# Performance work log

Hardware: AMD Instinct MI355X
Metric: run time of the kernel (lower is better)

## Reference

```python
import jax, jax.numpy as jnp
import numpy as np
from jax import lax

MAX_DECAY = 0.99
EPS = 1e-05
TOPK = 4


def ema_mask_group(moving_avg, new, mask, decay0, cluster_update_num):
    """Faithful port of ema_tensor_mask_group_inplace, including the quirk that
    the Python-level `decay` variable is carried (and possibly shrunk) across
    cluster iterations. Implemented as a lax.scan over clusters carrying decay.
    moving_avg/new: [C] or [C, D]; mask, cluster_update_num: [C].
    """
    def step(decay, xs):
        ma, nw, m, c = xs
        d = jnp.where((m != 0) & (c <= 10.0), decay * c / 10.0, decay)
        out = jnp.where(m != 0, ma * d + nw * (1.0 - d), ma)
        return d, out
    _, out = lax.scan(step, jnp.asarray(decay0, moving_avg.dtype),
                      (moving_avg, new, mask, cluster_update_num))
    return out


def laplace_smoothing(x, n_categories, eps=EPS):
    return (x + eps) / (x.sum() + n_categories * eps)


def setup_inputs() -> dict:
    key = jax.random.key(0)
    k1, k2 = jax.random.split(key)
    N, C, D = 65536, 512, 256
    return {
        "inputs_flatten": jax.random.normal(k1, (N, D), dtype=jnp.float32),
        "dictionary": jax.random.normal(k2, (C, D), dtype=jnp.float32),
        "cluster_size_sum": jnp.zeros((C,), dtype=jnp.float32),
        "cluster_value": jnp.zeros((C, D), dtype=jnp.float32),
        "cluster_update_num": jnp.ones((C,), dtype=jnp.float32),
    }


def reference(inputs_flatten, dictionary, cluster_size_sum, cluster_value,
              cluster_update_num):
    N, D = inputs_flatten.shape
    C = dictionary.shape[0]
    dic = lax.stop_gradient(dictionary)  # dictionary used via .detach()/.data

    # squared euclidean distances [N, C]
    distances = (jnp.sum(inputs_flatten ** 2, axis=1, keepdims=True)
                 + jnp.sum(dic ** 2, axis=1)
                 - 2.0 * jnp.matmul(inputs_flatten, dic.T))

    # ascending sort -> take topK smallest distances
    _, topk_idx = lax.top_k(-distances, TOPK)          # [N, K]
    topk_emb = dic[topk_idx]                            # [N, K, D]
    group_emb = jnp.sum(topk_emb, axis=1) / TOPK        # [N, D]

    # multi-hot encodings via scatter
    rows = jnp.arange(N)[:, None]
    encodings = jnp.zeros((N, C), dtype=jnp.float32).at[rows, topk_idx].set(1.0)

    # ---- training-mode EMA codebook update (single device: all_gather = identity) ----
    x_sg = lax.stop_gradient(inputs_flatten)
    cluster_size = jnp.sum(encodings, axis=0)           # [C]
    cluster_mask = (cluster_size != 0).astype(jnp.float32)
    cluster_update_num_new = cluster_update_num + cluster_mask

    cluster_size_sum_new = ema_mask_group(cluster_size_sum, cluster_size,
                                          cluster_mask, MAX_DECAY,
                                          cluster_update_num_new)
    input_sum = jnp.matmul(encodings.T, x_sg)           # [C, D]
    cluster_value_new = ema_mask_group(cluster_value, input_sum, cluster_mask,
                                       MAX_DECAY, cluster_update_num_new)

    cs = laplace_smoothing(cluster_size_sum_new, C, EPS) * cluster_size_sum_new.sum()
    embed_normalized = jnp.where(cluster_mask[:, None] == 1.0,
                                 cluster_value_new / cs[:, None],
                                 cluster_value_new)
    dictionary_new = embed_normalized                   # world_size == 1

    # straight-through estimator
    group_emb = lax.stop_gradient(group_emb - inputs_flatten) + inputs_flatten
    return (group_emb, topk_idx, dictionary_new, cluster_size_sum_new,
            cluster_value_new, cluster_update_num_new)
```

## Files before the change

kernel.cpp:

```cpp
#include <hip/hip_runtime.h>

#define N_ROWS 65536
#define C_CLUST 512
#define D_DIM 256

#define WS_DICTT   0
#define WS_DSQ     131072
#define WS_CS      197120
#define WS_DCY     197632
#define WS_ISUM    198144
#define WS_COUNTS  329216
#define WS_OFFSETS 329728
#define WS_FILL    330752
#define WS_ROWLIST 331264

#define OUT_GEMB 0
#define OUT_TOPK 16777216
#define OUT_DICT 17039360
#define OUT_CSS  17170432
#define OUT_CV   17170944
#define OUT_CNUM 17302016

#define RPB 128

typedef __attribute__((ext_vector_type(8))) short short8;
typedef __attribute__((ext_vector_type(16))) float f32x16;

__device__ __forceinline__ unsigned short f2bf(float v) {
    union { float f; unsigned u; } c; c.f = v;
    unsigned r = c.u + 0x7FFFu + ((c.u >> 16) & 1u);
    return (unsigned short)(r >> 16);
}
__device__ __forceinline__ float bf2f(unsigned short h) {
    union { float f; unsigned u; } c; c.u = ((unsigned)h) << 16;
    return c.f;
}

__global__ void zero_k(unsigned* counts, unsigned* fill, float* isum) {
    int t = blockIdx.x * blockDim.x + threadIdx.x;
    if (t < 512) { counts[t] = 0u; fill[t] = 0u; }
    if (t < C_CLUST * D_DIM) isum[t] = 0.f;
}

__global__ void prep_dict(const float* __restrict__ dic, float* __restrict__ ws) {
    int c = blockIdx.x, k = threadIdx.x;
    float v = dic[c * D_DIM + k];
    unsigned short* dhi = (unsigned short*)(ws + WS_DICTT);
    unsigned short* dlo = dhi + 131072;
    unsigned short hb = f2bf(v);
    dhi[c * D_DIM + k] = hb;
    dlo[c * D_DIM + k] = f2bf(__fsub_rn(v, bf2f(hb)));
    __shared__ float red[256];
    red[k] = v * v;
    __syncthreads();
    for (int s = 128; s > 0; s >>= 1) {
        if (k < s) red[k] += red[k + s];
        __syncthreads();
    }
    if (k == 0) ws[WS_DSQ + c] = red[0];
}

__global__ __launch_bounds__(256, 2) void stage1_cand(
    const float* __restrict__ x, const float* __restrict__ ws,
    float* __restrict__ cand_out)
{
    __shared__ unsigned short hlds[32 * 264];
    __shared__ unsigned short llds[32 * 264];
    __shared__ float dsq_s[512];

    const int tid = threadIdx.x;
    const int lane = tid & 63;
    const int w = tid >> 6;
    const int kg = lane >> 5;
    const int cl_lane = lane & 31;
    const int row = blockIdx.x * 128 + w * 32 + cl_lane;

    const unsigned short* dhi = (const unsigned short*)(ws + WS_DICTT);
    const unsigned short* dlo = dhi + 131072;

    for (int i = tid; i < 512; i += 256) dsq_s[i] = ws[WS_DSQ + i];

    short8 bhi[16], blo[16];
    #pragma unroll
    for (int s = 0; s < 16; ++s) {
        const float* px = &x[(size_t)row * D_DIM + s * 16 + kg * 8];
        float4 u0 = *reinterpret_cast<const float4*>(px);
        float4 u1 = *reinterpret_cast<const float4*>(px + 4);
        float vv[8] = {u0.x, u0.y, u0.z, u0.w, u1.x, u1.y, u1.z, u1.w};
        short8 h, l;
        #pragma unroll
        for (int e = 0; e < 8; ++e) {
            unsigned short hb = f2bf(vv[e]);
            unsigned short lb = f2bf(__fsub_rn(vv[e], bf2f(hb)));
            h[e] = (short)hb; l[e] = (short)lb;
        }
        bhi[s] = h; blo[s] = l;
    }

    unsigned long long kk[8];
    #pragma unroll
    for (int q = 0; q < 8; ++q) kk[q] = 0xFFFFFFFFFFFFFFFFULL;

    for (int ct = 0; ct < 16; ++ct) {
        __syncthreads();
        for (int q = tid; q < 1024; q += 256) {
            int c = q >> 5, k8 = (q & 31) * 8;
            *reinterpret_cast<uint4*>(&hlds[c * 264 + k8]) =
                *reinterpret_cast<const uint4*>(&dhi[(ct * 32 + c) * D_DIM + k8]);
            *reinterpret_cast<uint4*>(&llds[c * 264 + k8]) =
                *reinterpret_cast<const uint4*>(&dlo[(ct * 32 + c) * D_DIM + k8]);
        }
        __syncthreads();

        f32x16 ahh, ahl, alh;
        #pragma unroll
        for (int r = 0; r < 16; ++r) { ahh[r] = 0.f; ahl[r] = 0.f; alh[r] = 0.f; }

        #pragma unroll
        for (int s = 0; s < 16; ++s) {
            short8 Ah = *reinterpret_cast<const short8*>(
                &hlds[cl_lane * 264 + s * 16 + kg * 8]);
            short8 Al = *reinterpret_cast<const short8*>(
                &llds[cl_lane * 264 + s * 16 + kg * 8]);
            ahh = __builtin_amdgcn_mfma_f32_32x32x16_bf16(Ah, bhi[s], ahh, 0, 0, 0);
            ahl = __builtin_amdgcn_mfma_f32_32x32x16_bf16(Ah, blo[s], ahl, 0, 0, 0);
            alh = __builtin_amdgcn_mfma_f32_32x32x16_bf16(Al, bhi[s], alh, 0, 0, 0);
        }

        #pragma unroll
        for (int r = 0; r < 16; ++r) {
            int cl = ct * 32 + (r & 3) + 8 * (r >> 2) + 4 * kg;
            float dot = ahh[r] + ahl[r] + alh[r];
            float key = (dsq_s[cl] + 1024.0f) - 2.0f * dot;
            unsigned long long v =
                ((unsigned long long)__float_as_uint(key) << 32) | (unsigned)cl;
            #pragma unroll
            for (int q = 0; q < 8; ++q) {
                bool lt = v < kk[q];
                unsigned long long mn = lt ? v : kk[q];
                unsigned long long mx = lt ? kk[q] : v;
                kk[q] = mn; v = mx;
            }
        }
    }

    uint4 wv;
    wv.x = (unsigned)(kk[0] & 0xFFFF) | ((unsigned)(kk[1] & 0xFFFF) << 16);
    wv.y = (unsigned)(kk[2] & 0xFFFF) | ((unsigned)(kk[3] & 0xFFFF) << 16);
    wv.z = (unsigned)(kk[4] & 0xFFFF) | ((unsigned)(kk[5] & 0xFFFF) << 16);
    wv.w = (unsigned)(kk[6] & 0xFFFF) | ((unsigned)(kk[7] & 0xFFFF) << 16);
    *reinterpret_cast<uint4*>(&cand_out[(size_t)row * 256 + kg * 4]) = wv;
}

__global__ __launch_bounds__(256, 2) void refine_k(
    const float* __restrict__ x, const float* __restrict__ dic,
    const float* __restrict__ ws, float* __restrict__ out,
    unsigned* __restrict__ counts)
{
    extern __shared__ float smem[];
    float* xl  = smem;
    float* dl  = smem + 4 * 260;
    float* sqb = smem + 4 * 260 + 64 * 260;
    __shared__ float distb[64];
    __shared__ float xss[4];
    __shared__ int cidx[64];
    __shared__ int selp[16];

    const int t = threadIdx.x;
    const int rowBase = blockIdx.x * 4;
    const unsigned short* candp = (const unsigned short*)(out + OUT_GEMB);

    if (t < 64) cidx[t] = (int)candp[(size_t)(rowBase + (t >> 4)) * 512 + (t & 15)];

    {
        int r = t >> 6, seg = t & 63;
        const float* px = &x[(size_t)(rowBase + r) * D_DIM + seg * 4];
        float4 a = *reinterpret_cast<const float4*>(px);
        *reinterpret_cast<float4*>(&xl[r * 260 + seg * 4]) = a;
        sqb[r * 256 + seg * 4 + 0] = a.x * a.x;
        sqb[r * 256 + seg * 4 + 1] = a.y * a.y;
        sqb[r * 256 + seg * 4 + 2] = a.z * a.z;
        sqb[r * 256 + seg * 4 + 3] = a.w * a.w;
    }
    __syncthreads();

    {
        int r = t >> 6, g = t & 63;
        for (int st = 128; st > 0; st >>= 1) {
            for (int k = g; k < st; k += 64)
                sqb[r * 256 + k] += sqb[r * 256 + k + st];
            __syncthreads();
        }
        if (t < 4) xss[t] = sqb[t * 256];
    }
    __syncthreads();

    {
        int p = t >> 2, q = t & 3;
        const float* src = &dic[(size_t)cidx[p] * D_DIM + q * 64];
        #pragma unroll
        for (int i = 0; i < 16; ++i)
            *reinterpret_cast<float4*>(&dl[p * 260 + q * 64 + i * 4]) =
                *reinterpret_cast<const float4*>(src + i * 4);
    }
    __syncthreads();

    if (t < 64) {
        int r = t >> 4;
        float acc = 0.f;
        const float* dp = &dl[t * 260];
        const float* xp = &xl[r * 260];
        #pragma unroll 4
        for (int k4 = 0; k4 < 64; ++k4) {
            float4 dv = *reinterpret_cast<const float4*>(dp + k4 * 4);
            float4 xv = *reinterpret_cast<const float4*>(xp + k4 * 4);
            acc = fmaf(xv.x, dv.x, acc);
            acc = fmaf(xv.y, dv.y, acc);
            acc = fmaf(xv.z, dv.z, acc);
            acc = fmaf(xv.w, dv.w, acc);
        }
        float ds = ws[WS_DSQ + cidx[t]];
        distb[t] = __fsub_rn(__fadd_rn(xss[r], ds), __fmul_rn(2.0f, acc));
    }
    __syncthreads();

    if (t < 4) {
        float bv0 = 3.4e38f, bv1 = 3.4e38f, bv2 = 3.4e38f, bv3 = 3.4e38f;
        int bi0 = 0x7FFFFFFF, bi1 = 0x7FFFFFFF, bi2 = 0x7FFFFFFF, bi3 = 0x7FFFFFFF;
        int bp0 = 0, bp1 = 0, bp2 = 0, bp3 = 0;
        for (int s = 0; s < 16; ++s) {
            int p = t * 16 + s;
            float v = distb[p];
            int ci = cidx[p];
            if (v < bv3 || (v == bv3 && ci < bi3)) {
                if (v < bv2 || (v == bv2 && ci < bi2)) {
                    bv3 = bv2; bi3 = bi2; bp3 = bp2;
                    if (v < bv1 || (v == bv1 && ci < bi1)) {
                        bv2 = bv1; bi2 = bi1; bp2 = bp1;
                        if (v < bv0 || (v == bv0 && ci < bi0)) {
                            bv1 = bv0; bi1 = bi0; bp1 = bp0;
                            bv0 = v; bi0 = ci; bp0 = p;
                        } else { bv1 = v; bi1 = ci; bp1 = p; }
                    } else { bv2 = v; bi2 = ci; bp2 = p; }
                } else { bv3 = v; bi3 = ci; bp3 = p; }
            }
        }
        int row = rowBase + t;
        out[OUT_TOPK + (size_t)row * 4 + 0] = (float)bi0;
        out[OUT_TOPK + (size_t)row * 4 + 1] = (float)bi1;
        out[OUT_TOPK + (size_t)row * 4 + 2] = (float)bi2;
        out[OUT_TOPK + (size_t)row * 4 + 3] = (float)bi3;
        atomicAdd(&counts[bi0], 1u);
        atomicAdd(&counts[bi1], 1u);
        atomicAdd(&counts[bi2], 1u);
        atomicAdd(&counts[bi3], 1u);
        selp[t * 4 + 0] = bp0 & 63;
        selp[t * 4 + 1] = bp1 & 63;
        selp[t * 4 + 2] = bp2 & 63;
        selp[t * 4 + 3] = bp3 & 63;
    }
    __syncthreads();

    {
        int r = t >> 6, u = t & 63;
        int p0 = selp[r * 4 + 0], p1 = selp[r * 4 + 1];
        int p2 = selp[r * 4 + 2], p3 = selp[r * 4 + 3];
        int k4 = u * 4;
        float4 a = *reinterpret_cast<const float4*>(&dl[p0 * 260 + k4]);
        float4 b = *reinterpret_cast<const float4*>(&dl[p1 * 260 + k4]);
        float4 c = *reinterpret_cast<const float4*>(&dl[p2 * 260 + k4]);
        float4 e = *reinterpret_cast<const float4*>(&dl[p3 * 260 + k4]);
        float4 xv = *reinterpret_cast<const float4*>(&xl[r * 260 + k4]);
        float4 o;
        float g;
        g = __fmul_rn(__fadd_rn(__fadd_rn(__fadd_rn(a.x, b.x), c.x), e.x), 0.25f);
        o.x = __fadd_rn(__fsub_rn(g, xv.x), xv.x);
        g = __fmul_rn(__fadd_rn(__fadd_rn(__fadd_rn(a.y, b.y), c.y), e.y), 0.25f);
        o.y = __fadd_rn(__fsub_rn(g, xv.y), xv.y);
        g = __fmul_rn(__fadd_rn(__fadd_rn(__fadd_rn(a.z, b.z), c.z), e.z), 0.25f);
        o.z = __fadd_rn(__fsub_rn(g, xv.z), xv.z);
        g = __fmul_rn(__fadd_rn(__fadd_rn(__fadd_rn(a.w, b.w), c.w), e.w), 0.25f);
        o.w = __fadd_rn(__fsub_rn(g, xv.w), xv.w);
        *reinterpret_cast<float4*>(
            &out[OUT_GEMB + (size_t)(rowBase + r) * D_DIM + k4]) = o;
    }
}

__global__ void prefix_k(const unsigned* __restrict__ counts, unsigned* __restrict__ offsets) {
    __shared__ unsigned s[512];
    int t = threadIdx.x;
    unsigned my = counts[t];
    s[t] = my;
    __syncthreads();
    for (int off = 1; off < 512; off <<= 1) {
        unsigned v = (t >= off) ? s[t - off] : 0u;
        __syncthreads();
        s[t] += v;
        __syncthreads();
    }
    offsets[t] = s[t] - my;
    if (t == 511) offsets[512] = s[511];
}

__global__ void scatter_k(const float* __restrict__ topk, const unsigned* __restrict__ offsets,
                          unsigned* __restrict__ fill, unsigned* __restrict__ rowlist) {
    int row = blockIdx.x * 256 + threadIdx.x;
    #pragma unroll
    for (int k = 0; k < 4; ++k) {
        int c = (int)topk[row * 4 + k];
        unsigned p = atomicAdd(&fill[c], 1u);
        rowlist[offsets[c] + p] = ((unsigned)c << 16) | (unsigned)row;
    }
}

__global__ __launch_bounds__(256, 8) void cluster_sum2_k(
    const float* __restrict__ x, const unsigned* __restrict__ rowlist,
    float* __restrict__ isum)
{
    const int d = threadIdx.x;
    const int base = blockIdx.x * RPB;
    unsigned e0 = rowlist[base];
    int ccur = (int)(e0 >> 16);
    float acc = 0.f;
    #pragma unroll 4
    for (int j = 0; j < RPB; ++j) {
        unsigned e = rowlist[base + j];
        int c = (int)(e >> 16);
        float v = x[(e & 0xFFFFu) * D_DIM + d];
        if (c != ccur) {
            atomicAdd(&isum[ccur * D_DIM + d], acc);
            acc = 0.f;
            ccur = c;
        }
        acc += v;
    }
    atomicAdd(&isum[ccur * D_DIM + d], acc);
}

__global__ void ema_scalar_k(const float* __restrict__ css_in, const float* __restrict__ cnum_in,
                             const unsigned* __restrict__ counts,
                             float* __restrict__ ws, float* __restrict__ out) {
    __shared__ float sdecay[512];
    __shared__ float sred[512];
    __shared__ float scn[512];
    __shared__ unsigned smask[512];
    int t = threadIdx.x;
    unsigned cnt = counts[t];
    float size = (float)cnt;
    float mask = (cnt != 0u) ? 1.f : 0.f;
    float cnum_new = __fadd_rn(cnum_in[t], mask);
    scn[t] = cnum_new;
    smask[t] = cnt;
    __syncthreads();
    if (t == 0) {
        float d = 0.99f;
        for (int c = 0; c < 512; ++c) {
            if (smask[c] != 0u && scn[c] <= 10.0f)
                d = __fmul_rn(d, scn[c]) / 10.0f;
            sdecay[c] = d;
        }
    }
    __syncthreads();
    float d = sdecay[t];
    float css = css_in[t];
    float css_new = (cnt != 0u)
        ? __fadd_rn(__fmul_rn(css, d), __fmul_rn(size, __fsub_rn(1.f, d)))
        : css;
    out[OUT_CSS + t] = css_new;
    out[OUT_CNUM + t] = cnum_new;
    sred[t] = css_new;
    __syncthreads();
    for (int s = 256; s > 0; s >>= 1) {
        if (t < s) sred[t] += sred[t + s];
        __syncthreads();
    }
    float S = sred[0];
    float cs = __fmul_rn(__fdiv_rn(__fadd_rn(css_new, 1e-5f),
                                   __fadd_rn(S, 0.00512f)), S);
    ws[WS_CS + t] = cs;
    ws[WS_DCY + t] = d;
}

__global__ void final_k(const float* __restrict__ cv_in, const float* __restrict__ ws,
                        const unsigned* __restrict__ counts, float* __restrict__ out) {
    int c = blockIdx.x, d = threadIdx.x;
    float isum = ws[WS_ISUM + c * D_DIM + d];
    float dc = ws[WS_DCY + c];
    float cs = ws[WS_CS + c];
    unsigned cnt = counts[c];
    float cv = cv_in[c * D_DIM + d];
    float cvn = (cnt != 0u)
        ? __fadd_rn(__fmul_rn(cv, dc), __fmul_rn(isum, __fsub_rn(1.f, dc)))
        : cv;
    out[OUT_CV + c * D_DIM + d] = cvn;
    out[OUT_DICT + c * D_DIM + d] = (cnt != 0u) ? __fdiv_rn(cvn, cs) : cvn;
}

extern "C" void kernel_launch(void* const* d_in, const int* in_sizes, int n_in,
                              void* d_out, int out_size, void* d_ws, size_t ws_size,
                              hipStream_t stream) {
    const float* x       = (const float*)d_in[0];
    const float* dic     = (const float*)d_in[1];
    const float* css_in  = (const float*)d_in[2];
    const float* cv_in   = (const float*)d_in[3];
    const float* cnum_in = (const float*)d_in[4];
    float* out = (float*)d_out;
    float* ws  = (float*)d_ws;
    unsigned* counts  = (unsigned*)(ws + WS_COUNTS);
    unsigned* offsets = (unsigned*)(ws + WS_OFFSETS);
    unsigned* fill    = (unsigned*)(ws + WS_FILL);
    unsigned* rowlist = (unsigned*)(ws + WS_ROWLIST);

    zero_k<<<C_CLUST * D_DIM / 256, 256, 0, stream>>>(counts, fill, ws + WS_ISUM);
    prep_dict<<<C_CLUST, 256, 0, stream>>>(dic, ws);

    stage1_cand<<<N_ROWS / 128, 256, 0, stream>>>(x, ws, out + OUT_GEMB);

    size_t smem2 = (4 * 260 + 64 * 260 + 4 * 256) * sizeof(float);
    refine_k<<<N_ROWS / 4, 256, smem2, stream>>>(x, dic, ws, out, counts);

    prefix_k<<<1, 512, 0, stream>>>(counts, offsets);
    scatter_k<<<N_ROWS / 256, 256, 0, stream>>>(out + OUT_TOPK, offsets, fill, rowlist);
    cluster_sum2_k<<<N_ROWS * 4 / RPB, 256, 0, stream>>>(x, rowlist, ws + WS_ISUM);
    ema_scalar_k<<<1, 512, 0, stream>>>(css_in, cnum_in, counts, ws, out);
    final_k<<<C_CLUST, 256, 0, stream>>>(cv_in, ws, counts, out);
}
```

Measured before the change: 673.2 us.

## Restructure refine kernel to 16 rows per block with precomputed row norms

```diff
diff --git a/kernel.cpp b/kernel.cpp
--- a/kernel.cpp
+++ b/kernel.cpp
@@ -6,6 +6,7 @@
 
 #define WS_DICTT   0
 #define WS_DSQ     131072
+#define WS_XSQ     131584
 #define WS_CS      197120
 #define WS_DCY     197632
 #define WS_ISUM    198144
@@ -58,6 +59,19 @@
         __syncthreads();
     }
     if (k == 0) ws[WS_DSQ + c] = red[0];
+}
+
+__global__ void row_sq(const float* __restrict__ x, float* __restrict__ ws) {
+    int row = blockIdx.x, k = threadIdx.x;
+    float v = x[row * D_DIM + k];
+    __shared__ float red[256];
+    red[k] = v * v;
+    __syncthreads();
+    for (int s = 128; s > 0; s >>= 1) {
+        if (k < s) red[k] += red[k + s];
+        __syncthreads();
+    }
+    if (k == 0) ws[WS_XSQ + row] = red[0];
 }
 
 __global__ __launch_bounds__(256, 2) void stage1_cand(
@@ -152,65 +166,39 @@
     *reinterpret_cast<uint4*>(&cand_out[(size_t)row * 256 + kg * 4]) = wv;
 }
 
-__global__ __launch_bounds__(256, 2) void refine_k(
+__global__ __launch_bounds__(256, 4) void refine_k(
     const float* __restrict__ x, const float* __restrict__ dic,
     const float* __restrict__ ws, float* __restrict__ out,
     unsigned* __restrict__ counts)
 {
-    extern __shared__ float smem[];
-    float* xl  = smem;
-    float* dl  = smem + 4 * 260;
-    float* sqb = smem + 4 * 260 + 64 * 260;
-    __shared__ float distb[64];
-    __shared__ float xss[4];
-    __shared__ int cidx[64];
-    __shared__ int selp[16];
+    __shared__ float xl[16 * 260];
+    __shared__ float distb[256];
+    __shared__ int cidx[256];
+    __shared__ int seli[16 * 4];
 
     const int t = threadIdx.x;
-    const int rowBase = blockIdx.x * 4;
+    const int rowBase = blockIdx.x * 16;
     const unsigned short* candp = (const unsigned short*)(out + OUT_GEMB);
 
-    if (t < 64) cidx[t] = (int)candp[(size_t)(rowBase + (t >> 4)) * 512 + (t & 15)];
+    cidx[t] = (int)candp[(size_t)(rowBase + (t >> 4)) * 512 + (t & 15)];
+
+    #pragma unroll
+    for (int i = 0; i < 4; ++i) {
+        int q = t + i * 256;
+        int r = q >> 6, seg = q & 63;
+        *reinterpret_cast<float4*>(&xl[r * 260 + seg * 4]) =
+            *reinterpret_cast<const float4*>(
+                &x[(size_t)(rowBase + r) * D_DIM + seg * 4]);
+    }
+    __syncthreads();
 
     {
-        int r = t >> 6, seg = t & 63;
-        const float* px = &x[(size_t)(rowBase + r) * D_DIM + seg * 4];
-        float4 a = *reinterpret_cast<const float4*>(px);
-        *reinterpret_cast<float4*>(&xl[r * 260 + seg * 4]) = a;
-        sqb[r * 256 + seg * 4 + 0] = a.x * a.x;
-        sqb[r * 256 + seg * 4 + 1] = a.y * a.y;
-        sqb[r * 256 + seg * 4 + 2] = a.z * a.z;
-        sqb[r * 256 + seg * 4 + 3] = a.w * a.w;
-    }
-    __syncthreads();
-
-    {
-        int r = t >> 6, g = t & 63;
-        for (int st = 128; st > 0; st >>= 1) {
-            for (int k = g; k < st; k += 64)
-                sqb[r * 256 + k] += sqb[r * 256 + k + st];
-            __syncthreads();
-        }
-        if (t < 4) xss[t] = sqb[t * 256];
-    }
-    __syncthreads();
-
-    {
-        int p = t >> 2, q = t & 3;
-        const float* src = &dic[(size_t)cidx[p] * D_DIM + q * 64];
-        #pragma unroll
-        for (int i = 0; i < 16; ++i)
-            *reinterpret_cast<float4*>(&dl[p * 260 + q * 64 + i * 4]) =
-                *reinterpret_cast<const float4*>(src + i * 4);
-    }
-    __syncthreads();
-
-    if (t < 64) {
         int r = t >> 4;
+        int ci = cidx[t];
+        const float* dp = &dic[(size_t)ci * D_DIM];
+        const float* xp = &xl[r * 260];
         float acc = 0.f;
-        const float* dp = &dl[t * 260];
-        const float* xp = &xl[r * 260];
-        #pragma unroll 4
+        #pragma unroll 8
         for (int k4 = 0; k4 < 64; ++k4) {
             float4 dv = *reinterpret_cast<const float4*>(dp + k4 * 4);
             float4 xv = *reinterpret_cast<const float4*>(xp + k4 * 4);
@@ -219,30 +207,30 @@
             acc = fmaf(xv.z, dv.z, acc);
             acc = fmaf(xv.w, dv.w, acc);
         }
-        float ds = ws[WS_DSQ + cidx[t]];
-        distb[t] = __fsub_rn(__fadd_rn(xss[r], ds), __fmul_rn(2.0f, acc));
-    }
-    __syncthreads();
-
-    if (t < 4) {
+        float ds = ws[WS_DSQ + ci];
+        float xs = ws[WS_XSQ + rowBase + r];
+        distb[t] = __fsub_rn(__fadd_rn(xs, ds), __fmul_rn(2.0f, acc));
+    }
+    __syncthreads();
+
+    if (t < 16) {
         float bv0 = 3.4e38f, bv1 = 3.4e38f, bv2 = 3.4e38f, bv3 = 3.4e38f;
         int bi0 = 0x7FFFFFFF, bi1 = 0x7FFFFFFF, bi2 = 0x7FFFFFFF, bi3 = 0x7FFFFFFF;
-        int bp0 = 0, bp1 = 0, bp2 = 0, bp3 = 0;
         for (int s = 0; s < 16; ++s) {
             int p = t * 16 + s;
             float v = distb[p];
             int ci = cidx[p];
             if (v < bv3 || (v == bv3 && ci < bi3)) {
                 if (v < bv2 || (v == bv2 && ci < bi2)) {
-                    bv3 = bv2; bi3 = bi2; bp3 = bp2;
+                    bv3 = bv2; bi3 = bi2;
                     if (v < bv1 || (v == bv1 && ci < bi1)) {
-                        bv2 = bv1; bi2 = bi1; bp2 = bp1;
+                        bv2 = bv1; bi2 = bi1;
                         if (v < bv0 || (v == bv0 && ci < bi0)) {
-                            bv1 = bv0; bi1 = bi0; bp1 = bp0;
-                            bv0 = v; bi0 = ci; bp0 = p;
-                        } else { bv1 = v; bi1 = ci; bp1 = p; }
-                    } else { bv2 = v; bi2 = ci; bp2 = p; }
-                } else { bv3 = v; bi3 = ci; bp3 = p; }
+                            bv1 = bv0; bi1 = bi0;
+                            bv0 = v; bi0 = ci;
+                        } else { bv1 = v; bi1 = ci; }
+                    } else { bv2 = v; bi2 = ci; }
+                } else { bv3 = v; bi3 = ci; }
             }
         }
         int row = rowBase + t;
@@ -254,35 +242,38 @@
         atomicAdd(&counts[bi1], 1u);
         atomicAdd(&counts[bi2], 1u);
         atomicAdd(&counts[bi3], 1u);
-        selp[t * 4 + 0] = bp0 & 63;
-        selp[t * 4 + 1] = bp1 & 63;
-        selp[t * 4 + 2] = bp2 & 63;
-        selp[t * 4 + 3] = bp3 & 63;
+        seli[t * 4 + 0] = bi0;
+        seli[t * 4 + 1] = bi1;
+        seli[t * 4 + 2] = bi2;
+        seli[t * 4 + 3] = bi3;
     }
     __syncthreads();
 
     {
-        int r = t >> 6, u = t & 63;
-        int p0 = selp[r * 4 + 0], p1 = selp[r * 4 + 1];
-        int p2 = selp[r * 4 + 2], p3 = selp[r * 4 + 3];
-        int k4 = u * 4;
-        float4 a = *reinterpret_cast<const float4*>(&dl[p0 * 260 + k4]);
-        float4 b = *reinterpret_cast<const float4*>(&dl[p1 * 260 + k4]);
-        float4 c = *reinterpret_cast<const float4*>(&dl[p2 * 260 + k4]);
-        float4 e = *reinterpret_cast<const float4*>(&dl[p3 * 260 + k4]);
-        float4 xv = *reinterpret_cast<const float4*>(&xl[r * 260 + k4]);
-        float4 o;
-        float g;
-        g = __fmul_rn(__fadd_rn(__fadd_rn(__fadd_rn(a.x, b.x), c.x), e.x), 0.25f);
-        o.x = __fadd_rn(__fsub_rn(g, xv.x), xv.x);
-        g = __fmul_rn(__fadd_rn(__fadd_rn(__fadd_rn(a.y, b.y), c.y), e.y), 0.25f);
-        o.y = __fadd_rn(__fsub_rn(g, xv.y), xv.y);
-        g = __fmul_rn(__fadd_rn(__fadd_rn(__fadd_rn(a.z, b.z), c.z), e.z), 0.25f);
-        o.z = __fadd_rn(__fsub_rn(g, xv.z), xv.z);
-        g = __fmul_rn(__fadd_rn(__fadd_rn(__fadd_rn(a.w, b.w), c.w), e.w), 0.25f);
-        o.w = __fadd_rn(__fsub_rn(g, xv.w), xv.w);
-        *reinterpret_cast<float4*>(
-            &out[OUT_GEMB + (size_t)(rowBase + r) * D_DIM + k4]) = o;
+        int r = t >> 4, u = t & 15;
+        int p0 = seli[r * 4 + 0], p1 = seli[r * 4 + 1];
+        int p2 = seli[r * 4 + 2], p3 = seli[r * 4 + 3];
+        #pragma unroll
+        for (int h = 0; h < 4; ++h) {
+            int k4 = u * 16 + h * 4;
+            float4 a = *reinterpret_cast<const float4*>(&dic[(size_t)p0 * D_DIM + k4]);
+            float4 b = *reinterpret_cast<const float4*>(&dic[(size_t)p1 * D_DIM + k4]);
+            float4 c = *reinterpret_cast<const float4*>(&dic[(size_t)p2 * D_DIM + k4]);
+            float4 e = *reinterpret_cast<const float4*>(&dic[(size_t)p3 * D_DIM + k4]);
+            float4 xv = *reinterpret_cast<const float4*>(&xl[r * 260 + k4]);
+            float4 o;
+            float g;
+            g = __fmul_rn(__fadd_rn(__fadd_rn(__fadd_rn(a.x, b.x), c.x), e.x), 0.25f);
+            o.x = __fadd_rn(__fsub_rn(g, xv.x), xv.x);
+            g = __fmul_rn(__fadd_rn(__fadd_rn(__fadd_rn(a.y, b.y), c.y), e.y), 0.25f);
+            o.y = __fadd_rn(__fsub_rn(g, xv.y), xv.y);
+            g = __fmul_rn(__fadd_rn(__fadd_rn(__fadd_rn(a.z, b.z), c.z), e.z), 0.25f);
+            o.z = __fadd_rn(__fsub_rn(g, xv.z), xv.z);
+            g = __fmul_rn(__fadd_rn(__fadd_rn(__fadd_rn(a.w, b.w), c.w), e.w), 0.25f);
+            o.w = __fadd_rn(__fsub_rn(g, xv.w), xv.w);
+            *reinterpret_cast<float4*>(
+                &out[OUT_GEMB + (size_t)(rowBase + r) * D_DIM + k4]) = o;
+        }
     }
 }
 
@@ -413,11 +404,11 @@
 
     zero_k<<<C_CLUST * D_DIM / 256, 256, 0, stream>>>(counts, fill, ws + WS_ISUM);
     prep_dict<<<C_CLUST, 256, 0, stream>>>(dic, ws);
+    row_sq<<<N_ROWS, 256, 0, stream>>>(x, ws);
 
     stage1_cand<<<N_ROWS / 128, 256, 0, stream>>>(x, ws, out + OUT_GEMB);
 
-    size_t smem2 = (4 * 260 + 64 * 260 + 4 * 256) * sizeof(float);
-    refine_k<<<N_ROWS / 4, 256, smem2, stream>>>(x, dic, ws, out, counts);
+    refine_k<<<N_ROWS / 16, 256, 0, stream>>>(x, dic, ws, out, counts);
 
     prefix_k<<<1, 512, 0, stream>>>(counts, offsets);
     scatter_k<<<N_ROWS / 256, 256, 0, stream>>>(out + OUT_TOPK, offsets, fill, rowlist);
```

Result: faster. 649.4 us (-3.5%).
